# Optimization experiments

Hardware: AMD Instinct MI355X
Metric: run time of the kernel (lower is better)

Reference implementation:

```python
import jax, jax.numpy as jnp
import numpy as np

B, N, D, T = 4, 512, 128, 1000

def setup_inputs() -> dict:
    key = jax.random.key(0)
    ks = jax.random.split(key, 8)
    s = 0.02  # init scale
    return {
        "adj_noisy": jax.random.randint(ks[0], (B, N, N), 0, 2, dtype=jnp.int32),
        "t": jax.random.randint(ks[1], (B,), 0, T + 1, dtype=jnp.int32),
        "time_embed": jax.random.normal(ks[2], (T + 1, D), dtype=jnp.float32) * s,
        "no_cond_embed": jnp.zeros((D,), dtype=jnp.float32),
        "edge_embed": jax.random.normal(ks[3], (2, D), dtype=jnp.float32) * s,
        "W1": jax.random.normal(ks[4], (3 * D, D), dtype=jnp.float32) * s,
        "b1": jnp.zeros((D,), dtype=jnp.float32),
        "W2": jax.random.normal(ks[5], (D, D), dtype=jnp.float32) * s,
        "b2": jnp.zeros((D,), dtype=jnp.float32),
        "Wc": jax.random.normal(ks[6], (2 * D, 2), dtype=jnp.float32) * s,
        "bc": jnp.zeros((2,), dtype=jnp.float32),
    }


def reference(adj_noisy, t, time_embed, no_cond_embed, edge_embed, W1, b1, W2, b2, Wc, bc):
    d = time_embed.shape[1]
    b, n, _ = adj_noisy.shape
    # time embedding broadcast to [B, N, D]
    t_emb = jnp.broadcast_to(time_embed[t][:, None, :], (b, n, d))
    # encode_noisy_graph: mean over j of edge_embed[adj[b,i,j]]. Since adj in {0,1},
    # mean of gathered rows == (1-p)*E[0] + p*E[1] with p = fraction of ones (exact same math).
    p = adj_noisy.astype(jnp.float32).mean(axis=2)  # [B, N]
    H_noisy = (1.0 - p)[..., None] * edge_embed[0] + p[..., None] * edge_embed[1]
    # uncond path: H_prev = no_cond_embed broadcast
    H_prev = jnp.broadcast_to(no_cond_embed[None, None, :], (b, n, d))
    # fusion MLP on [B, N, 3D]
    x = jnp.concatenate([H_noisy, H_prev, t_emb], axis=-1)
    h = jax.nn.relu(jnp.einsum('bnf,fd->bnd', x, W1) + b1)
    H_fused = jax.nn.relu(jnp.einsum('bnd,de->bne', h, W2) + b2)
    # edge classifier on concat([H_i, H_j]): split Wc so we never materialize [B,N,N,2D].
    li = jnp.einsum('bnd,dc->bnc', H_fused, Wc[:d])  # contribution of H_i
    lj = jnp.einsum('bnd,dc->bnc', H_fused, Wc[d:])  # contribution of H_j
    logits = li[:, :, None, :] + lj[:, None, :, :] + bc  # [B, N, N, 2]
    return logits
```

## Files before the change

### kernel.cpp

```cpp
#include <hip/hip_runtime.h>

#define DD 128
#define NN 512

__global__ __launch_bounds__(512) void rows_kernel(
    const int* __restrict__ adj,
    const int* __restrict__ tt,
    const float* __restrict__ time_embed,
    const float* __restrict__ no_cond,
    const float* __restrict__ edge_embed,
    const float* __restrict__ W1,
    const float* __restrict__ b1,
    const float* __restrict__ W2,
    const float* __restrict__ b2,
    const float* __restrict__ Wc,
    const float* __restrict__ bc,
    float* __restrict__ ws_li,
    float* __restrict__ ws_lj)
{
    __shared__ float sP[8 * 8 * DD];
    __shared__ float s_part[512];
    __shared__ float s_cb[DD];
    __shared__ float s_v1[DD];
    __shared__ float s_p[8];

    const int t = threadIdx.x;
    const int lane = t & 63;
    const int wv = t >> 6;
    const int row0 = blockIdx.x * 8;
    const int b = blockIdx.x >> 6;

    const int4* abase = (const int4*)(adj + (size_t)(row0 + wv) * NN);
    int4 a0 = abase[lane];
    int4 a1 = abase[lane + 64];

    {
        const int d = t & 127;
        const int q = t >> 7;
        float c = 0.f;
        if (q == 0) {
            const float* wp = W1 + d;
#pragma unroll 8
            for (int k = 0; k < 128; ++k)
                c = fmaf(edge_embed[k], wp[k * DD], c);
        } else if (q == 1) {
            const float* wp = W1 + 128 * DD + d;
#pragma unroll 8
            for (int k = 0; k < 128; ++k)
                c = fmaf(no_cond[k], wp[k * DD], c);
        } else if (q == 2) {
            const float* teb = time_embed + (size_t)tt[b] * DD;
            const float* wp = W1 + 256 * DD + d;
#pragma unroll 8
            for (int k = 0; k < 128; ++k)
                c = fmaf(teb[k], wp[k * DD], c);
        } else {
            const float* wp = W1 + d;
#pragma unroll 8
            for (int k = 0; k < 128; ++k)
                c = fmaf(edge_embed[DD + k] - edge_embed[k], wp[k * DD], c);
        }
        s_part[t] = c;
    }

    {
        int s = a0.x + a0.y + a0.z + a0.w + a1.x + a1.y + a1.z + a1.w;
#pragma unroll
        for (int off = 32; off; off >>= 1) s += __shfl_xor(s, off, 64);
        if (lane == 0) s_p[wv] = (float)s * (1.0f / (float)NN);
    }
    __syncthreads();

    if (t < DD) {
        s_cb[t] = s_part[t] + s_part[t + 128] + s_part[t + 256] + b1[t];
        s_v1[t] = s_part[t + 384];
    }
    __syncthreads();

    float p[8];
#pragma unroll
    for (int r = 0; r < 8; ++r) p[r] = s_p[r];

    const int cg = t & 63;
    const int dh = t >> 6;
    const int c0 = cg * 2;
    float acc[8][2];
#pragma unroll
    for (int r = 0; r < 8; ++r) { acc[r][0] = 0.f; acc[r][1] = 0.f; }

    const float2* W2v = (const float2*)W2;
#pragma unroll
    for (int i = 0; i < 16; ++i) {
        const int d = dh * 16 + i;
        float2 w = W2v[(d * DD + c0) >> 1];
        float cbd = s_cb[d];
        float v1d = s_v1[d];
#pragma unroll
        for (int r = 0; r < 8; ++r) {
            float h = fmaxf(fmaf(p[r], v1d, cbd), 0.f);
            acc[r][0] = fmaf(h, w.x, acc[r][0]);
            acc[r][1] = fmaf(h, w.y, acc[r][1]);
        }
    }
#pragma unroll
    for (int r = 0; r < 8; ++r)
        *(float2*)&sP[(r * 8 + dh) * DD + c0] = make_float2(acc[r][0], acc[r][1]);
    __syncthreads();

    float s0 = 0.f, s1 = 0.f;
#pragma unroll
    for (int k = 0; k < 8; ++k) {
        const float* rowp = &sP[(wv * 8 + k) * DD];
        s0 += rowp[lane];
        s1 += rowp[lane + 64];
    }
    float f0 = fmaxf(s0 + b2[lane], 0.f);
    float f1 = fmaxf(s1 + b2[lane + 64], 0.f);

    const float2* Wc2 = (const float2*)Wc;
    float2 wa0 = Wc2[lane];
    float2 wa1 = Wc2[lane + 64];
    float2 wb0 = Wc2[DD + lane];
    float2 wb1 = Wc2[DD + lane + 64];

    float li0 = f0 * wa0.x + f1 * wa1.x;
    float li1 = f0 * wa0.y + f1 * wa1.y;
    float lj0 = f0 * wb0.x + f1 * wb1.x;
    float lj1 = f0 * wb0.y + f1 * wb1.y;

#pragma unroll
    for (int off = 32; off; off >>= 1) {
        li0 += __shfl_xor(li0, off, 64);
        li1 += __shfl_xor(li1, off, 64);
        lj0 += __shfl_xor(lj0, off, 64);
        lj1 += __shfl_xor(lj1, off, 64);
    }
    if (lane == 0) {
        int row = row0 + wv;
        *(float2*)&ws_li[row * 2] = make_float2(li0 + bc[0], li1 + bc[1]);
        *(float2*)&ws_lj[row * 2] = make_float2(lj0, lj1);
    }
}

__global__ __launch_bounds__(256) void write_kernel(
    const float* __restrict__ ws_li,
    const float* __restrict__ ws_lj,
    float* __restrict__ out)
{
    const int blk = blockIdx.x;
    const int t = threadIdx.x;
    const int b = blk >> 8;
    const int i = (blk & 255) * 2 + (t >> 7);
    const int j0 = (t & 127) * 4;

    float2 li = *(const float2*)&ws_li[(b * NN + i) * 2];
    float a0 = li.x;
    float a1 = li.y;

    float4 L0 = *(const float4*)&ws_lj[(b * NN + j0) * 2];
    float4 L1 = *(const float4*)&ws_lj[(b * NN + j0 + 2) * 2];

    float4 o0 = make_float4(a0 + L0.x, a1 + L0.y, a0 + L0.z, a1 + L0.w);
    float4 o1 = make_float4(a0 + L1.x, a1 + L1.y, a0 + L1.z, a1 + L1.w);

    size_t base = (((size_t)(b * NN + i)) * NN + j0) * 2;
    *(float4*)&out[base]     = o0;
    *(float4*)&out[base + 4] = o1;
}

extern "C" void kernel_launch(void* const* d_in, const int* in_sizes, int n_in,
                              void* d_out, int out_size, void* d_ws, size_t ws_size,
                              hipStream_t stream) {
    const int*   adj = (const int*)d_in[0];
    const int*   tt  = (const int*)d_in[1];
    const float* te  = (const float*)d_in[2];
    const float* nc  = (const float*)d_in[3];
    const float* ee  = (const float*)d_in[4];
    const float* W1  = (const float*)d_in[5];
    const float* b1  = (const float*)d_in[6];
    const float* W2  = (const float*)d_in[7];
    const float* b2  = (const float*)d_in[8];
    const float* Wc  = (const float*)d_in[9];
    const float* bc  = (const float*)d_in[10];
    float* out = (float*)d_out;

    float* ws    = (float*)d_ws;
    float* ws_li = ws;
    float* ws_lj = ws + 4096;

    rows_kernel<<<256, 512, 0, stream>>>(adj, tt, te, nc, ee, W1, b1, W2, b2,
                                         Wc, bc, ws_li, ws_lj);
    write_kernel<<<1024, 256, 0, stream>>>(ws_li, ws_lj, out);
}
```

Baseline: 88.06 us.

## Fuse row and write kernels into one cooperative kernel with grid sync

Measured after the change: 217.4 us. 2.47x slower.

```diff
diff --git a/kernel.cpp b/kernel.cpp
--- a/kernel.cpp
+++ b/kernel.cpp
@@ -1,9 +1,12 @@
 #include <hip/hip_runtime.h>
+#include <hip/hip_cooperative_groups.h>
+
+namespace cg = cooperative_groups;
 
 #define DD 128
 #define NN 512
 
-__global__ __launch_bounds__(512) void rows_kernel(
+__global__ __launch_bounds__(512) void fused_kernel(
     const int* __restrict__ adj,
     const int* __restrict__ tt,
     const float* __restrict__ time_embed,
@@ -15,52 +18,53 @@
     const float* __restrict__ b2,
     const float* __restrict__ Wc,
     const float* __restrict__ bc,
-    float* __restrict__ ws_li,
-    float* __restrict__ ws_lj)
+    float* __restrict__ out,
+    float* __restrict__ ws_lj,
+    float* __restrict__ ws_part)
 {
     __shared__ float sP[8 * 8 * DD];
-    __shared__ float s_part[512];
+    __shared__ float sRA[512];
+    __shared__ float sRB[512];
     __shared__ float s_cb[DD];
     __shared__ float s_v1[DD];
     __shared__ float s_p[8];
+    __shared__ float s_li[16];
 
     const int t = threadIdx.x;
     const int lane = t & 63;
     const int wv = t >> 6;
-    const int row0 = blockIdx.x * 8;
-    const int b = blockIdx.x >> 6;
-
-    const int4* abase = (const int4*)(adj + (size_t)(row0 + wv) * NN);
+    const int bl = blockIdx.x;
+    const int b = bl >> 6;
+    const int kc = bl & 63;
+
+    cg::grid_group grid = cg::this_grid();
+
+    const int4* abase = (const int4*)(adj + (size_t)(bl * 8 + wv) * NN);
     int4 a0 = abase[lane];
     int4 a1 = abase[lane + 64];
 
     {
         const int d = t & 127;
-        const int q = t >> 7;
-        float c = 0.f;
-        if (q == 0) {
-            const float* wp = W1 + d;
-#pragma unroll 8
-            for (int k = 0; k < 128; ++k)
-                c = fmaf(edge_embed[k], wp[k * DD], c);
-        } else if (q == 1) {
-            const float* wp = W1 + 128 * DD + d;
-#pragma unroll 8
-            for (int k = 0; k < 128; ++k)
-                c = fmaf(no_cond[k], wp[k * DD], c);
-        } else if (q == 2) {
+        const int s = t >> 7;
+        const int vr0 = kc * 8 + s * 2;
+        float acc;
+        if (vr0 < 128) {
+            acc = edge_embed[vr0] * W1[vr0 * DD + d];
+            acc = fmaf(edge_embed[vr0 + 1], W1[(vr0 + 1) * DD + d], acc);
+        } else if (vr0 < 256) {
+            acc = no_cond[vr0 - 128] * W1[vr0 * DD + d];
+            acc = fmaf(no_cond[vr0 - 127], W1[(vr0 + 1) * DD + d], acc);
+        } else if (vr0 < 384) {
             const float* teb = time_embed + (size_t)tt[b] * DD;
-            const float* wp = W1 + 256 * DD + d;
-#pragma unroll 8
-            for (int k = 0; k < 128; ++k)
-                c = fmaf(teb[k], wp[k * DD], c);
+            acc = teb[vr0 - 256] * W1[vr0 * DD + d];
+            acc = fmaf(teb[vr0 - 255], W1[(vr0 + 1) * DD + d], acc);
         } else {
-            const float* wp = W1 + d;
-#pragma unroll 8
-            for (int k = 0; k < 128; ++k)
-                c = fmaf(edge_embed[DD + k] - edge_embed[k], wp[k * DD], c);
-        }
-        s_part[t] = c;
+            const int k = vr0 - 384;
+            acc = (edge_embed[DD + k] - edge_embed[k]) * W1[k * DD + d];
+            acc = fmaf(edge_embed[DD + k + 1] - edge_embed[k + 1],
+                       W1[(k + 1) * DD + d], acc);
+        }
+        sRA[t] = acc;
     }
 
     {
@@ -70,10 +74,29 @@
         if (lane == 0) s_p[wv] = (float)s * (1.0f / (float)NN);
     }
     __syncthreads();
-
+    if (t < DD)
+        ws_part[(b * 64 + kc) * DD + t] =
+            sRA[t] + sRA[t + 128] + sRA[t + 256] + sRA[t + 384];
+
+    __threadfence();
+    grid.sync();
+
+    {
+        const int d = t & 127;
+        const int g = t >> 7;
+        const float* base = ws_part + (size_t)b * 64 * DD;
+        float sc = 0.f, sv = 0.f;
+#pragma unroll
+        for (int m = 0; m < 12; ++m) sc += base[(g * 12 + m) * DD + d];
+#pragma unroll
+        for (int m = 0; m < 4; ++m)  sv += base[(48 + g * 4 + m) * DD + d];
+        sRA[t] = sc;
+        sRB[t] = sv;
+    }
+    __syncthreads();
     if (t < DD) {
-        s_cb[t] = s_part[t] + s_part[t + 128] + s_part[t + 256] + b1[t];
-        s_v1[t] = s_part[t + 384];
+        s_cb[t] = sRA[t] + sRA[t + 128] + sRA[t + 256] + sRA[t + 384] + b1[t];
+        s_v1[t] = sRB[t] + sRB[t + 128] + sRB[t + 256] + sRB[t + 384];
     }
     __syncthreads();
 
@@ -81,9 +104,9 @@
 #pragma unroll
     for (int r = 0; r < 8; ++r) p[r] = s_p[r];
 
-    const int cg = t & 63;
+    const int cg_ = t & 63;
     const int dh = t >> 6;
-    const int c0 = cg * 2;
+    const int c0 = cg_ * 2;
     float acc[8][2];
 #pragma unroll
     for (int r = 0; r < 8; ++r) { acc[r][0] = 0.f; acc[r][1] = 0.f; }
@@ -107,65 +130,62 @@
         *(float2*)&sP[(r * 8 + dh) * DD + c0] = make_float2(acc[r][0], acc[r][1]);
     __syncthreads();
 
-    float s0 = 0.f, s1 = 0.f;
-#pragma unroll
-    for (int k = 0; k < 8; ++k) {
-        const float* rowp = &sP[(wv * 8 + k) * DD];
-        s0 += rowp[lane];
-        s1 += rowp[lane + 64];
-    }
-    float f0 = fmaxf(s0 + b2[lane], 0.f);
-    float f1 = fmaxf(s1 + b2[lane + 64], 0.f);
-
-    const float2* Wc2 = (const float2*)Wc;
-    float2 wa0 = Wc2[lane];
-    float2 wa1 = Wc2[lane + 64];
-    float2 wb0 = Wc2[DD + lane];
-    float2 wb1 = Wc2[DD + lane + 64];
-
-    float li0 = f0 * wa0.x + f1 * wa1.x;
-    float li1 = f0 * wa0.y + f1 * wa1.y;
-    float lj0 = f0 * wb0.x + f1 * wb1.x;
-    float lj1 = f0 * wb0.y + f1 * wb1.y;
-
-#pragma unroll
-    for (int off = 32; off; off >>= 1) {
-        li0 += __shfl_xor(li0, off, 64);
-        li1 += __shfl_xor(li1, off, 64);
-        lj0 += __shfl_xor(lj0, off, 64);
-        lj1 += __shfl_xor(lj1, off, 64);
-    }
-    if (lane == 0) {
-        int row = row0 + wv;
-        *(float2*)&ws_li[row * 2] = make_float2(li0 + bc[0], li1 + bc[1]);
-        *(float2*)&ws_lj[row * 2] = make_float2(lj0, lj1);
-    }
-}
-
-__global__ __launch_bounds__(256) void write_kernel(
-    const float* __restrict__ ws_li,
-    const float* __restrict__ ws_lj,
-    float* __restrict__ out)
-{
-    const int blk = blockIdx.x;
-    const int t = threadIdx.x;
-    const int b = blk >> 8;
-    const int i = (blk & 255) * 2 + (t >> 7);
-    const int j0 = (t & 127) * 4;
-
-    float2 li = *(const float2*)&ws_li[(b * NN + i) * 2];
-    float a0 = li.x;
-    float a1 = li.y;
-
-    float4 L0 = *(const float4*)&ws_lj[(b * NN + j0) * 2];
-    float4 L1 = *(const float4*)&ws_lj[(b * NN + j0 + 2) * 2];
-
-    float4 o0 = make_float4(a0 + L0.x, a1 + L0.y, a0 + L0.z, a1 + L0.w);
-    float4 o1 = make_float4(a0 + L1.x, a1 + L1.y, a0 + L1.z, a1 + L1.w);
-
-    size_t base = (((size_t)(b * NN + i)) * NN + j0) * 2;
-    *(float4*)&out[base]     = o0;
-    *(float4*)&out[base + 4] = o1;
+    {
+        float s0 = 0.f, s1 = 0.f;
+#pragma unroll
+        for (int k = 0; k < 8; ++k) {
+            const float* rowp = &sP[(wv * 8 + k) * DD];
+            s0 += rowp[lane];
+            s1 += rowp[lane + 64];
+        }
+        float f0 = fmaxf(s0 + b2[lane], 0.f);
+        float f1 = fmaxf(s1 + b2[lane + 64], 0.f);
+
+        const float2* Wc2 = (const float2*)Wc;
+        float2 wa0 = Wc2[lane];
+        float2 wa1 = Wc2[lane + 64];
+        float2 wb0 = Wc2[DD + lane];
+        float2 wb1 = Wc2[DD + lane + 64];
+
+        float li0 = f0 * wa0.x + f1 * wa1.x;
+        float li1 = f0 * wa0.y + f1 * wa1.y;
+        float lj0 = f0 * wb0.x + f1 * wb1.x;
+        float lj1 = f0 * wb0.y + f1 * wb1.y;
+
+#pragma unroll
+        for (int off = 32; off; off >>= 1) {
+            li0 += __shfl_xor(li0, off, 64);
+            li1 += __shfl_xor(li1, off, 64);
+            lj0 += __shfl_xor(lj0, off, 64);
+            lj1 += __shfl_xor(lj1, off, 64);
+        }
+        if (lane == 0) {
+            *(float2*)&ws_lj[(bl * 8 + wv) * 2] = make_float2(lj0, lj1);
+            s_li[wv * 2]     = li0 + bc[0];
+            s_li[wv * 2 + 1] = li1 + bc[1];
+        }
+    }
+
+    __threadfence();
+    grid.sync();
+
+    {
+        const int r = t >> 6;
+        const int j0 = lane * 8;
+        const float la = s_li[r * 2];
+        const float lb = s_li[r * 2 + 1];
+        const float* ljp = ws_lj + ((size_t)b * NN + j0) * 2;
+        float4 L0 = *(const float4*)(ljp + 0);
+        float4 L1 = *(const float4*)(ljp + 4);
+        float4 L2 = *(const float4*)(ljp + 8);
+        float4 L3 = *(const float4*)(ljp + 12);
+
+        size_t base = ((size_t)(bl * 8 + r) * NN + j0) * 2;
+        *(float4*)&out[base + 0]  = make_float4(la + L0.x, lb + L0.y, la + L0.z, lb + L0.w);
+        *(float4*)&out[base + 4]  = make_float4(la + L1.x, lb + L1.y, la + L1.z, lb + L1.w);
+        *(float4*)&out[base + 8]  = make_float4(la + L2.x, lb + L2.y, la + L2.z, lb + L2.w);
+        *(float4*)&out[base + 12] = make_float4(la + L3.x, lb + L3.y, la + L3.z, lb + L3.w);
+    }
 }
 
 extern "C" void kernel_launch(void* const* d_in, const int* in_sizes, int n_in,
@@ -184,11 +204,12 @@
     const float* bc  = (const float*)d_in[10];
     float* out = (float*)d_out;
 
-    float* ws    = (float*)d_ws;
-    float* ws_li = ws;
-    float* ws_lj = ws + 4096;
-
-    rows_kernel<<<256, 512, 0, stream>>>(adj, tt, te, nc, ee, W1, b1, W2, b2,
-                                         Wc, bc, ws_li, ws_lj);
-    write_kernel<<<1024, 256, 0, stream>>>(ws_li, ws_lj, out);
+    float* ws      = (float*)d_ws;
+    float* ws_lj   = ws;
+    float* ws_part = ws + 4096;
+
+    void* args[] = {&adj, &tt, &te, &nc, &ee, &W1, &b1, &W2, &b2, &Wc, &bc,
+                    &out, &ws_lj, &ws_part};
+    hipLaunchCooperativeKernel((const void*)fused_kernel, dim3(256), dim3(512),
+                               args, 0, stream);
 }
```
